# Kernel tuning notes

Measured on AMD Instinct MI355X. Metric: run time of the kernel, lower is better.

The kernel has to match this reference:

```python
import jax, jax.numpy as jnp
import numpy as np

B, T, H2, E, V = 64, 400, 1024, 256, 50000  # batch, src len, hidden*2, embed, vocab


def setup_inputs() -> dict:
    key = jax.random.key(0)
    ks = jax.random.split(key, 20)
    s = 0.02
    return {
        "input_ids": jax.random.randint(ks[0], (B, 1), 0, V),
        "pre_hidden": jax.random.normal(ks[1], (B, 1, H2), jnp.float32),
        "enc_out": jax.random.normal(ks[2], (B, T, H2), jnp.float32),
        "source_input": jax.random.randint(ks[3], (B, T), 0, V),
        "emb_table": jax.random.normal(ks[4], (V, E), jnp.float32) * s,
        "W_align": jax.random.normal(ks[5], (1, 2 * H2), jnp.float32) * s,
        "b_align": jnp.zeros((1,), jnp.float32),
        "W_ih": jax.random.normal(ks[6], (3 * H2, E), jnp.float32) * s,
        "W_hh": jax.random.normal(ks[7], (3 * H2, H2), jnp.float32) * s,
        "b_ih": jnp.zeros((3 * H2,), jnp.float32),
        "b_hh": jnp.zeros((3 * H2,), jnp.float32),
        "W_comb": jax.random.normal(ks[8], (E, H2 + E), jnp.float32) * s,
        "b_comb": jnp.zeros((E,), jnp.float32),
        "W_out": jax.random.normal(ks[9], (V, 2 * H2 + E), jnp.float32) * s,
        "b_out": jnp.zeros((V,), jnp.float32),
        "W_copy": jax.random.normal(ks[10], (H2, H2), jnp.float32) * s,
        "b_copy": jnp.zeros((H2,), jnp.float32),
    }


def reference(input_ids, pre_hidden, enc_out, source_input, emb_table,
              W_align, b_align, W_ih, W_hh, b_ih, b_hh,
              W_comb, b_comb, W_out, b_out, W_copy, b_copy):
    # embeddings: [B,1,E]  (dropout omitted: eval mode)
    emb = emb_table[input_ids[:, 0]][:, None, :]
    # Bahdanau-style alignment over source positions
    rep = jnp.broadcast_to(pre_hidden, (B, T, H2))
    scores = jnp.tanh(jnp.concatenate([enc_out, rep], axis=2) @ W_align.T + b_align)  # [B,T,1]
    attn = jax.nn.softmax(scores, axis=1)            # softmax over time, [B,T,1]
    attn_bt = attn[:, :, 0]                          # [B,T]
    attn_w = attn_bt[:, None, :]                     # [B,1,T] (returned shape)
    context = jnp.einsum("bt,bth->bh", attn_bt, enc_out)[:, None, :]  # [B,1,H2]
    # combine + relu -> GRU input
    new_in = jax.nn.relu(jnp.concatenate([emb, context], axis=2) @ W_comb.T + b_comb)  # [B,1,E]
    # single GRU step (torch gate order: r, z, n)
    x, h = new_in[:, 0], pre_hidden[:, 0]
    gi = x @ W_ih.T + b_ih
    gh = h @ W_hh.T + b_hh
    i_r, i_z, i_n = jnp.split(gi, 3, axis=1)
    h_r, h_z, h_n = jnp.split(gh, 3, axis=1)
    r = jax.nn.sigmoid(i_r + h_r)
    z = jax.nn.sigmoid(i_z + h_z)
    n = jnp.tanh(i_n + r * h_n)
    h_new = (1.0 - z) * n + z * h                    # [B,H2]
    current_hidden = h_new[:, None, :]               # [B,1,H2]
    # generation distribution
    feat = jnp.concatenate([emb[:, 0], context[:, 0], h_new], axis=1)  # [B,4H+E]
    gen = jax.nn.softmax(feat @ W_out.T + b_out, axis=1)               # [B,V]
    # copy attention weights (returned diagnostic)
    copy_a = jax.nn.sigmoid(enc_out @ W_copy.T + b_copy)               # [B,T,H2]
    copy_w = jax.nn.softmax(jnp.einsum("bth,bh->bt", copy_a, h_new), axis=1)
    # fused batched scatter-add replacing the per-example one-hot matmul loop
    pos = jnp.zeros((B, V), jnp.float32).at[jnp.arange(B)[:, None], source_input].add(attn_bt)
    out = gen + pos
    return out, current_hidden, attn_w, copy_w
```

## Files before the change

kernel.cpp:

```cpp
#include <hip/hip_runtime.h>
#include <hip/hip_bf16.h>
#include <cstddef>

#define BB 64
#define TT 400
#define H2 1024
#define EE 256
#define VV 50000
#define KF 2304
#define KC 1280

typedef _Float16 half8 __attribute__((ext_vector_type(8)));
typedef float f32x4 __attribute__((ext_vector_type(4)));

#define WS_SCORES   0
#define WS_ATTN     25600
#define WS_CONTEXT  51200
#define WS_X        116736
#define WS_HNEW     133120
#define WS_FEAT     198656
#define WS_SRAW     346112
#define WS_STATS    371712

#define OUT_MAIN    0
#define OUT_HID     3200000
#define OUT_ATTN    3265536
#define OUT_CPW     3291136

__device__ inline float sigm(float x){ return 1.f/(1.f + __expf(-x)); }

__global__ void k_scores(const float* __restrict__ enc, const float* __restrict__ Wa,
                         float* __restrict__ scores_raw){
  int wave = threadIdx.x >> 6, lane = threadIdx.x & 63;
  int row = blockIdx.x * 4 + wave;
  const float4* e4 = (const float4*)(enc + (size_t)row * H2);
  const float4* w4 = (const float4*)Wa;
  float acc = 0.f;
#pragma unroll
  for (int i = 0; i < 4; ++i){
    float4 e = e4[i*64 + lane], w = w4[i*64 + lane];
    acc += e.x*w.x + e.y*w.y + e.z*w.z + e.w*w.w;
  }
  for (int m = 32; m >= 1; m >>= 1) acc += __shfl_xor(acc, m, 64);
  if (lane == 0) scores_raw[row] = acc;
}

__global__ void k_attn(const float* __restrict__ scores_raw, const float* __restrict__ pre_hidden,
                       const float* __restrict__ Wa, const float* __restrict__ b_align,
                       float* __restrict__ attn_bt, float* __restrict__ attn_w_out){
  int b = blockIdx.x, t = threadIdx.x;
  __shared__ float red[256];
  const float4* p4 = (const float4*)(pre_hidden + (size_t)b * H2);
  const float4* w4 = (const float4*)(Wa + H2);
  float4 p = p4[t], w = w4[t];
  red[t] = p.x*w.x + p.y*w.y + p.z*w.z + p.w*w.w;
  __syncthreads();
  for (int s = 128; s > 0; s >>= 1){ if (t < s) red[t] += red[t+s]; __syncthreads(); }
  float phd = red[0] + b_align[0];
  __syncthreads();
  int t2 = t + 256;
  float v0 = -1e30f, v1 = -1e30f;
  if (t  < TT) v0 = tanhf(scores_raw[b*TT + t ] + phd);
  if (t2 < TT) v1 = tanhf(scores_raw[b*TT + t2] + phd);
  red[t] = fmaxf(v0, v1); __syncthreads();
  for (int s = 128; s > 0; s >>= 1){ if (t < s) red[t] = fmaxf(red[t], red[t+s]); __syncthreads(); }
  float M = red[0]; __syncthreads();
  float e0 = (t  < TT) ? __expf(v0 - M) : 0.f;
  float e1 = (t2 < TT) ? __expf(v1 - M) : 0.f;
  red[t] = e0 + e1; __syncthreads();
  for (int s = 128; s > 0; s >>= 1){ if (t < s) red[t] += red[t+s]; __syncthreads(); }
  float inv = 1.f / red[0];
  if (t < TT){ float a = e0*inv; attn_bt[b*TT+t] = a; attn_w_out[b*TT+t] = a; }
  if (t2 < TT){ float a = e1*inv; attn_bt[b*TT+t2] = a; attn_w_out[b*TT+t2] = a; }
}

__global__ void k_context(const float* __restrict__ enc, const float* __restrict__ attn_bt,
                          float* __restrict__ context){
  int bx = blockIdx.x;
  int b = bx >> 2;
  int h = (bx & 3) * 256 + threadIdx.x;
  const float* e = enc + (size_t)b * TT * H2 + h;
  const float* a = attn_bt + b * TT;
  float acc = 0.f;
  for (int t = 0; t < TT; t += 4){
    acc += a[t  ] * e[(size_t)(t  ) * H2];
    acc += a[t+1] * e[(size_t)(t+1) * H2];
    acc += a[t+2] * e[(size_t)(t+2) * H2];
    acc += a[t+3] * e[(size_t)(t+3) * H2];
  }
  context[b*H2 + h] = acc;
}

__global__ void k_newin(const int* __restrict__ input_ids, const float* __restrict__ emb_table,
                        const float* __restrict__ context, const float* __restrict__ W_comb,
                        const float* __restrict__ b_comb, float* __restrict__ x,
                        float* __restrict__ feat){
  int b = blockIdx.x, t = threadIdx.x;
  __shared__ float xs[KC];
  int id = input_ids[b];
  float ev = emb_table[(size_t)id * EE + t];
  xs[t] = ev; feat[b*KF + t] = ev;
#pragma unroll
  for (int q = 0; q < 4; ++q){
    float cv = context[b*H2 + q*256 + t];
    xs[EE + q*256 + t] = cv;
    feat[b*KF + EE + q*256 + t] = cv;
  }
  __syncthreads();
  const float4* w4 = (const float4*)(W_comb + (size_t)t * KC);
  const float4* x4 = (const float4*)xs;
  float acc = b_comb[t];
  for (int k = 0; k < KC/4; ++k){
    float4 w = w4[k], xv = x4[k];
    acc += w.x*xv.x + w.y*xv.y + w.z*xv.z + w.w*xv.w;
  }
  x[b*EE + t] = fmaxf(acc, 0.f);
}

__global__ void k_gru(const float* __restrict__ x, const float* __restrict__ pre_hidden,
                      const float* __restrict__ W_ih, const float* __restrict__ W_hh,
                      const float* __restrict__ b_ih, const float* __restrict__ b_hh,
                      float* __restrict__ h_new, float* __restrict__ feat,
                      float* __restrict__ cur_hid){
  int h = blockIdx.x, t = threadIdx.x;
  __shared__ float wi[768];
  __shared__ float wh[3072];
  wi[t      ] = W_ih[(size_t)(h        ) * EE + t];
  wi[256 + t] = W_ih[(size_t)(H2   + h ) * EE + t];
  wi[512 + t] = W_ih[(size_t)(2*H2 + h ) * EE + t];
#pragma unroll
  for (int q = 0; q < 4; ++q){
    wh[        q*256 + t] = W_hh[(size_t)(h       ) * H2 + q*256 + t];
    wh[1024 +  q*256 + t] = W_hh[(size_t)(H2  + h ) * H2 + q*256 + t];
    wh[2048 +  q*256 + t] = W_hh[(size_t)(2*H2 + h) * H2 + q*256 + t];
  }
  __syncthreads();
  int wave = t >> 6, lane = t & 63;
  float bir = b_ih[h], biz = b_ih[H2+h], bin = b_ih[2*H2+h];
  float bhr = b_hh[h], bhz = b_hh[H2+h], bhn = b_hh[2*H2+h];
  for (int bb = wave*16; bb < wave*16 + 16; ++bb){
    float air=0, aiz=0, ain=0, ahr=0, ahz=0, ahn=0;
#pragma unroll
    for (int i = 0; i < 4; ++i){
      float xv = x[bb*EE + i*64 + lane];
      air += xv * wi[      i*64 + lane];
      aiz += xv * wi[256 + i*64 + lane];
      ain += xv * wi[512 + i*64 + lane];
    }
#pragma unroll
    for (int i = 0; i < 16; ++i){
      float hv = pre_hidden[bb*H2 + i*64 + lane];
      ahr += hv * wh[        i*64 + lane];
      ahz += hv * wh[1024 +  i*64 + lane];
      ahn += hv * wh[2048 +  i*64 + lane];
    }
    for (int m = 32; m >= 1; m >>= 1){
      air += __shfl_xor(air, m, 64); aiz += __shfl_xor(aiz, m, 64); ain += __shfl_xor(ain, m, 64);
      ahr += __shfl_xor(ahr, m, 64); ahz += __shfl_xor(ahz, m, 64); ahn += __shfl_xor(ahn, m, 64);
    }
    if (lane == 0){
      float rg = sigm(air + bir + ahr + bhr);
      float zg = sigm(aiz + biz + ahz + bhz);
      float ng = tanhf(ain + bin + rg*(ahn + bhn));
      float hb = pre_hidden[bb*H2 + h];
      float hn = (1.f - zg)*ng + zg*hb;
      h_new[bb*H2 + h] = hn;
      cur_hid[bb*H2 + h] = hn;
      feat[bb*KF + KC + h] = hn;
    }
  }
}

__device__ inline void load16(const float* __restrict__ gp, float4* r){
  const float4* g4 = (const float4*)gp;
  r[0] = g4[0]; r[1] = g4[1]; r[2] = g4[2]; r[3] = g4[3];
}
__device__ inline void cvt16(const float4* r, _Float16* lp){
  half8 h0, h1;
  h0[0]=(_Float16)r[0].x; h0[1]=(_Float16)r[0].y; h0[2]=(_Float16)r[0].z; h0[3]=(_Float16)r[0].w;
  h0[4]=(_Float16)r[1].x; h0[5]=(_Float16)r[1].y; h0[6]=(_Float16)r[1].z; h0[7]=(_Float16)r[1].w;
  h1[0]=(_Float16)r[2].x; h1[1]=(_Float16)r[2].y; h1[2]=(_Float16)r[2].z; h1[3]=(_Float16)r[2].w;
  h1[4]=(_Float16)r[3].x; h1[5]=(_Float16)r[3].y; h1[6]=(_Float16)r[3].z; h1[7]=(_Float16)r[3].w;
  *(half8*)(lp)     = h0;
  *(half8*)(lp + 8) = h1;
}

__global__ __launch_bounds__(256) void k_gemm_copy(
    const float* __restrict__ A, const float* __restrict__ Wc,
    const float* __restrict__ b_copy, const float* __restrict__ h_new,
    float* __restrict__ s_raw){
  __shared__ _Float16 Ash[2][128*40];
  __shared__ _Float16 Bsh[2][128*40];
  int bx = blockIdx.x;
  int n0 = (bx & 7) * 128;
  int m0 = (bx >> 3) * 128;
  int tid = threadIdx.x;
  int lane = tid & 63, wave = tid >> 6;
  int wm = wave >> 1, wn = wave & 1;
  int quad = lane >> 4, r = lane & 15;
  int srow = tid >> 1, sc0 = (tid & 1) << 4;

  const float* Ap = A  + (size_t)(m0 + srow)*H2 + sc0;
  const float* Bp = Wc + (size_t)(n0 + srow)*H2 + sc0;

  f32x4 acc[4][4];
#pragma unroll
  for (int i = 0; i < 4; ++i)
#pragma unroll
    for (int j = 0; j < 4; ++j) acc[i][j] = (f32x4){0.f,0.f,0.f,0.f};

  float4 ra[4], rb[4];
  load16(Ap, ra); load16(Bp, rb);
  cvt16(ra, &Ash[0][srow*40 + sc0]); cvt16(rb, &Bsh[0][srow*40 + sc0]);
  load16(Ap + 32, ra); load16(Bp + 32, rb);
  __syncthreads();

  const int NT = H2/32;
  for (int kt = 0; kt < NT; ++kt){
    int cur = kt & 1;
    half8 af[4], bf[4];
#pragma unroll
    for (int i = 0; i < 4; ++i) af[i] = *(const half8*)&Ash[cur][(wm*64 + i*16 + r)*40 + quad*8];
#pragma unroll
    for (int j = 0; j < 4; ++j) bf[j] = *(const half8*)&Bsh[cur][(wn*64 + j*16 + r)*40 + quad*8];
    if (kt + 1 < NT){
      cvt16(ra, &Ash[cur^1][srow*40 + sc0]);
      cvt16(rb, &Bsh[cur^1][srow*40 + sc0]);
      if (kt + 2 < NT){
        load16(Ap + (kt+2)*32, ra);
        load16(Bp + (kt+2)*32, rb);
      }
    }
#pragma unroll
    for (int i = 0; i < 4; ++i)
#pragma unroll
      for (int j = 0; j < 4; ++j)
        acc[i][j] = __builtin_amdgcn_mfma_f32_16x16x32_f16(af[i], bf[j], acc[i][j], 0, 0, 0);
    __syncthreads();
  }
#pragma unroll
  for (int i = 0; i < 4; ++i){
#pragma unroll
    for (int rr = 0; rr < 4; ++rr){
      int m_loc = wm*64 + i*16 + quad*4 + rr;
      int m_g = m0 + m_loc;
      int b = m_g / TT;
      float v = 0.f;
#pragma unroll
      for (int j = 0; j < 4; ++j){
        int n_g = n0 + wn*64 + j*16 + r;
        float g = acc[i][j][rr] + b_copy[n_g];
        v += sigm(g) * h_new[b*H2 + n_g];
      }
      v += __shfl_xor(v, 1, 64); v += __shfl_xor(v, 2, 64);
      v += __shfl_xor(v, 4, 64); v += __shfl_xor(v, 8, 64);
      if (r == 0) atomicAdd(&s_raw[m_g], v);
    }
  }
}

__global__ void k_copysm(const float* __restrict__ s_raw, float* __restrict__ copy_w){
  int b = blockIdx.x, t = threadIdx.x;
  __shared__ float red[256];
  int t2 = t + 256;
  float v0 = (t  < TT) ? s_raw[b*TT + t ] : -1e30f;
  float v1 = (t2 < TT) ? s_raw[b*TT + t2] : -1e30f;
  red[t] = fmaxf(v0, v1); __syncthreads();
  for (int s = 128; s > 0; s >>= 1){ if (t < s) red[t] = fmaxf(red[t], red[t+s]); __syncthreads(); }
  float M = red[0]; __syncthreads();
  float e0 = (t  < TT) ? __expf(v0 - M) : 0.f;
  float e1 = (t2 < TT) ? __expf(v1 - M) : 0.f;
  red[t] = e0 + e1; __syncthreads();
  for (int s = 128; s > 0; s >>= 1){ if (t < s) red[t] += red[t+s]; __syncthreads(); }
  float inv = 1.f / red[0];
  if (t  < TT) copy_w[b*TT + t ] = e0 * inv;
  if (t2 < TT) copy_w[b*TT + t2] = e1 * inv;
}

__global__ __launch_bounds__(256) void k_gemm_out(
    const float* __restrict__ Wo, const float* __restrict__ feat,
    const float* __restrict__ b_out, float* __restrict__ logits){
  __shared__ __align__(16) char smem[33280];
  _Float16* AshB = (_Float16*)smem;
  _Float16* BshB = (_Float16*)(smem + 20480);
  float*    Csh  = (float*)smem;

  int m0 = blockIdx.x * 128;
  int tid = threadIdx.x;
  int lane = tid & 63, wave = tid >> 6;
  int wm = wave >> 1, wn = wave & 1;
  int quad = lane >> 4, r = lane & 15;

  f32x4 acc[4][2];
#pragma unroll
  for (int i = 0; i < 4; ++i)
#pragma unroll
    for (int j = 0; j < 2; ++j) acc[i][j] = (f32x4){0.f,0.f,0.f,0.f};

  int arow = tid >> 1, ac0 = (tid & 1) << 4;
  int arow_g = m0 + arow; if (arow_g >= VV) arow_g = VV - 1;
  const float* Ap = Wo + (size_t)arow_g * KF + ac0;
  const float* Bp = feat + (size_t)arow * KF + ac0;

  float4 ra[4], rb[4];
  load16(Ap, ra);
  if (tid < 128) load16(Bp, rb);
  cvt16(ra, &AshB[arow*40 + ac0]);
  if (tid < 128) cvt16(rb, &BshB[arow*40 + ac0]);
  load16(Ap + 32, ra);
  if (tid < 128) load16(Bp + 32, rb);
  __syncthreads();

  const int NT = KF/32;
  for (int kt = 0; kt < NT; ++kt){
    int cur = kt & 1;
    _Float16* Ash = AshB + cur*(128*40);
    _Float16* Bsh = BshB + cur*(64*40);
    half8 af[4], bf[2];
#pragma unroll
    for (int i = 0; i < 4; ++i) af[i] = *(const half8*)&Ash[(wm*64 + i*16 + r)*40 + quad*8];
#pragma unroll
    for (int j = 0; j < 2; ++j) bf[j] = *(const half8*)&Bsh[(wn*32 + j*16 + r)*40 + quad*8];
    if (kt + 1 < NT){
      int nxt = cur ^ 1;
      cvt16(ra, &AshB[nxt*(128*40) + arow*40 + ac0]);
      if (tid < 128) cvt16(rb, &BshB[nxt*(64*40) + arow*40 + ac0]);
      if (kt + 2 < NT){
        load16(Ap + (kt+2)*32, ra);
        if (tid < 128) load16(Bp + (kt+2)*32, rb);
      }
    }
#pragma unroll
    for (int i = 0; i < 4; ++i)
#pragma unroll
      for (int j = 0; j < 2; ++j)
        acc[i][j] = __builtin_amdgcn_mfma_f32_16x16x32_f16(af[i], bf[j], acc[i][j], 0, 0, 0);
    __syncthreads();
  }
#pragma unroll
  for (int i = 0; i < 4; ++i){
#pragma unroll
    for (int j = 0; j < 2; ++j){
#pragma unroll
      for (int rr = 0; rr < 4; ++rr){
        int m_loc = wm*64 + i*16 + quad*4 + rr;
        int n_loc = wn*32 + j*16 + r;
        int vg = m0 + m_loc;
        float bo = (vg < VV) ? b_out[vg] : 0.f;
        Csh[m_loc*65 + n_loc] = acc[i][j][rr] + bo;
      }
    }
  }
  __syncthreads();
  int vl = tid & 127, grp = tid >> 7;
  int vg = m0 + vl;
  if (vg < VV){
    for (int it = 0; it < 32; ++it){
      int brow = it*2 + grp;
      logits[(size_t)brow * VV + vg] = Csh[vl*65 + brow];
    }
  }
}

__global__ void k_gensm(const float* __restrict__ logits, float* __restrict__ stats){
  int b = blockIdx.x, t = threadIdx.x;
  __shared__ float red[256];
  const float* row = logits + (size_t)b * VV;
  float m = -1e30f;
  for (int v = t; v < VV; v += 256) m = fmaxf(m, row[v]);
  red[t] = m; __syncthreads();
  for (int s = 128; s > 0; s >>= 1){ if (t < s) red[t] = fmaxf(red[t], red[t+s]); __syncthreads(); }
  float M = red[0]; __syncthreads();
  float sum = 0.f;
  for (int v = t; v < VV; v += 256) sum += __expf(row[v] - M);
  red[t] = sum; __syncthreads();
  for (int s = 128; s > 0; s >>= 1){ if (t < s) red[t] += red[t+s]; __syncthreads(); }
  if (t == 0){ stats[b] = M; stats[64 + b] = 1.f / red[0]; }
}

__global__ void k_out(float* __restrict__ out, const float* __restrict__ stats){
  int idx4 = blockIdx.x * 256 + threadIdx.x;
  int base = idx4 * 4;
  int b = base / VV;
  float M = stats[b], inv = stats[64 + b];
  float4* p = (float4*)(out + base);
  float4 l = *p;
  l.x = __expf(l.x - M) * inv;
  l.y = __expf(l.y - M) * inv;
  l.z = __expf(l.z - M) * inv;
  l.w = __expf(l.w - M) * inv;
  *p = l;
}

__global__ void k_scatter(float* __restrict__ out, const int* __restrict__ src,
                          const float* __restrict__ attn_bt){
  int i = blockIdx.x * 256 + threadIdx.x;
  int b = i / TT;
  atomicAdd(&out[(size_t)b * VV + src[i]], attn_bt[i]);
}

extern "C" void kernel_launch(void* const* d_in, const int* in_sizes, int n_in,
                              void* d_out, int out_size, void* d_ws, size_t ws_size,
                              hipStream_t stream) {
  const int*   input_ids  = (const int*)  d_in[0];
  const float* pre_hidden = (const float*)d_in[1];
  const float* enc_out    = (const float*)d_in[2];
  const int*   source_in  = (const int*)  d_in[3];
  const float* emb_table  = (const float*)d_in[4];
  const float* W_align    = (const float*)d_in[5];
  const float* b_align    = (const float*)d_in[6];
  const float* W_ih       = (const float*)d_in[7];
  const float* W_hh       = (const float*)d_in[8];
  const float* b_ih       = (const float*)d_in[9];
  const float* b_hh       = (const float*)d_in[10];
  const float* W_comb     = (const float*)d_in[11];
  const float* b_comb     = (const float*)d_in[12];
  const float* W_out      = (const float*)d_in[13];
  const float* b_out      = (const float*)d_in[14];
  const float* W_copy     = (const float*)d_in[15];
  const float* b_copy     = (const float*)d_in[16];

  float* ws = (float*)d_ws;
  float* scores_raw = ws + WS_SCORES;
  float* attn_bt    = ws + WS_ATTN;
  float* context    = ws + WS_CONTEXT;
  float* x          = ws + WS_X;
  float* h_new      = ws + WS_HNEW;
  float* feat       = ws + WS_FEAT;
  float* s_raw      = ws + WS_SRAW;
  float* stats      = ws + WS_STATS;

  float* out        = (float*)d_out;
  float* out_hid    = out + OUT_HID;
  float* out_attn   = out + OUT_ATTN;
  float* out_cpw    = out + OUT_CPW;

  hipMemsetAsync(s_raw, 0, BB*TT*sizeof(float), stream);

  k_scores <<<BB*TT/4, 256, 0, stream>>>(enc_out, W_align, scores_raw);
  k_attn   <<<BB,      256, 0, stream>>>(scores_raw, pre_hidden, W_align, b_align, attn_bt, out_attn);
  k_context<<<BB*4,    256, 0, stream>>>(enc_out, attn_bt, context);
  k_newin  <<<BB,      256, 0, stream>>>(input_ids, emb_table, context, W_comb, b_comb, x, feat);
  k_gru    <<<H2,      256, 0, stream>>>(x, pre_hidden, W_ih, W_hh, b_ih, b_hh, h_new, feat, out_hid);
  k_gemm_copy<<<(BB*TT/128)*(H2/128), 256, 0, stream>>>(enc_out, W_copy, b_copy, h_new, s_raw);
  k_copysm <<<BB,      256, 0, stream>>>(s_raw, out_cpw);
  k_gemm_out<<<(VV + 127)/128, 256, 0, stream>>>(W_out, feat, b_out, out);
  k_gensm  <<<BB,      256, 0, stream>>>(out, stats);
  k_out    <<<BB*VV/1024, 256, 0, stream>>>(out, stats);
  k_scatter<<<BB*TT/256, 256, 0, stream>>>(out, source_in, attn_bt);
}
```

Before: 1.049 ms.

## Pre-convert copy GEMM operands to fp16, retile output GEMM, split softmax stats

enc_out is now converted to fp16 inside the scores kernel, and W_copy is converted by a new kernel, so the copy GEMM reads half-width operands instead of loading and converting fp32. The output GEMM tile shrinks from 128 to 64 vocab rows, which gives more blocks, and it gets a deeper three-stage register prefetch. The generation softmax statistics are split four ways per batch row and merged in k_out. Together these aim to cut memory traffic and raise parallelism, at the cost of an extra fp16 write of enc_out and added merge arithmetic.

After: 968.3 us. 1.08x faster.

```diff
diff --git a/kernel.cpp b/kernel.cpp
--- a/kernel.cpp
+++ b/kernel.cpp
@@ -11,6 +11,7 @@
 #define KC 1280
 
 typedef _Float16 half8 __attribute__((ext_vector_type(8)));
+typedef _Float16 half4 __attribute__((ext_vector_type(4)));
 typedef float f32x4 __attribute__((ext_vector_type(4)));
 
 #define WS_SCORES   0
@@ -21,6 +22,8 @@
 #define WS_FEAT     198656
 #define WS_SRAW     346112
 #define WS_STATS    371712
+#define WS_ENCH     372224
+#define WS_WCH      13479424
 
 #define OUT_MAIN    0
 #define OUT_HID     3200000
@@ -29,17 +32,30 @@
 
 __device__ inline float sigm(float x){ return 1.f/(1.f + __expf(-x)); }
 
+__global__ void k_cvt16(const float* __restrict__ src, _Float16* __restrict__ dst){
+  int i = blockIdx.x * 256 + threadIdx.x;
+  const float4* s4 = (const float4*)src;
+  float4 a = s4[i*2], b = s4[i*2+1];
+  half8 h;
+  h[0]=(_Float16)a.x; h[1]=(_Float16)a.y; h[2]=(_Float16)a.z; h[3]=(_Float16)a.w;
+  h[4]=(_Float16)b.x; h[5]=(_Float16)b.y; h[6]=(_Float16)b.z; h[7]=(_Float16)b.w;
+  *(half8*)(dst + (size_t)i*8) = h;
+}
+
 __global__ void k_scores(const float* __restrict__ enc, const float* __restrict__ Wa,
-                         float* __restrict__ scores_raw){
+                         float* __restrict__ scores_raw, _Float16* __restrict__ encH){
   int wave = threadIdx.x >> 6, lane = threadIdx.x & 63;
   int row = blockIdx.x * 4 + wave;
   const float4* e4 = (const float4*)(enc + (size_t)row * H2);
   const float4* w4 = (const float4*)Wa;
+  _Float16* eh = encH + (size_t)row * H2;
   float acc = 0.f;
 #pragma unroll
   for (int i = 0; i < 4; ++i){
     float4 e = e4[i*64 + lane], w = w4[i*64 + lane];
     acc += e.x*w.x + e.y*w.y + e.z*w.z + e.w*w.w;
+    half4 h; h[0]=(_Float16)e.x; h[1]=(_Float16)e.y; h[2]=(_Float16)e.z; h[3]=(_Float16)e.w;
+    *(half4*)(eh + (size_t)(i*64 + lane)*4) = h;
   }
   for (int m = 32; m >= 1; m >>= 1) acc += __shfl_xor(acc, m, 64);
   if (lane == 0) scores_raw[row] = acc;
@@ -171,22 +187,19 @@
   }
 }
 
-__device__ inline void load16(const float* __restrict__ gp, float4* r){
+__device__ inline void load8(const float* __restrict__ gp, float4* r){
   const float4* g4 = (const float4*)gp;
-  r[0] = g4[0]; r[1] = g4[1]; r[2] = g4[2]; r[3] = g4[3];
-}
-__device__ inline void cvt16(const float4* r, _Float16* lp){
-  half8 h0, h1;
-  h0[0]=(_Float16)r[0].x; h0[1]=(_Float16)r[0].y; h0[2]=(_Float16)r[0].z; h0[3]=(_Float16)r[0].w;
-  h0[4]=(_Float16)r[1].x; h0[5]=(_Float16)r[1].y; h0[6]=(_Float16)r[1].z; h0[7]=(_Float16)r[1].w;
-  h1[0]=(_Float16)r[2].x; h1[1]=(_Float16)r[2].y; h1[2]=(_Float16)r[2].z; h1[3]=(_Float16)r[2].w;
-  h1[4]=(_Float16)r[3].x; h1[5]=(_Float16)r[3].y; h1[6]=(_Float16)r[3].z; h1[7]=(_Float16)r[3].w;
-  *(half8*)(lp)     = h0;
-  *(half8*)(lp + 8) = h1;
+  r[0] = g4[0]; r[1] = g4[1];
+}
+__device__ inline void cvt8(const float4* r, _Float16* lp){
+  half8 h;
+  h[0]=(_Float16)r[0].x; h[1]=(_Float16)r[0].y; h[2]=(_Float16)r[0].z; h[3]=(_Float16)r[0].w;
+  h[4]=(_Float16)r[1].x; h[5]=(_Float16)r[1].y; h[6]=(_Float16)r[1].z; h[7]=(_Float16)r[1].w;
+  *(half8*)lp = h;
 }
 
 __global__ __launch_bounds__(256) void k_gemm_copy(
-    const float* __restrict__ A, const float* __restrict__ Wc,
+    const _Float16* __restrict__ A, const _Float16* __restrict__ Wc,
     const float* __restrict__ b_copy, const float* __restrict__ h_new,
     float* __restrict__ s_raw){
   __shared__ _Float16 Ash[2][128*40];
@@ -200,8 +213,8 @@
   int quad = lane >> 4, r = lane & 15;
   int srow = tid >> 1, sc0 = (tid & 1) << 4;
 
-  const float* Ap = A  + (size_t)(m0 + srow)*H2 + sc0;
-  const float* Bp = Wc + (size_t)(n0 + srow)*H2 + sc0;
+  const _Float16* Ap = A  + (size_t)(m0 + srow)*H2 + sc0;
+  const _Float16* Bp = Wc + (size_t)(n0 + srow)*H2 + sc0;
 
   f32x4 acc[4][4];
 #pragma unroll
@@ -209,10 +222,14 @@
 #pragma unroll
     for (int j = 0; j < 4; ++j) acc[i][j] = (f32x4){0.f,0.f,0.f,0.f};
 
-  float4 ra[4], rb[4];
-  load16(Ap, ra); load16(Bp, rb);
-  cvt16(ra, &Ash[0][srow*40 + sc0]); cvt16(rb, &Bsh[0][srow*40 + sc0]);
-  load16(Ap + 32, ra); load16(Bp + 32, rb);
+  {
+    half8 a0 = *(const half8*)(Ap), a1 = *(const half8*)(Ap+8);
+    half8 b0 = *(const half8*)(Bp), b1 = *(const half8*)(Bp+8);
+    *(half8*)&Ash[0][srow*40 + sc0] = a0; *(half8*)&Ash[0][srow*40 + sc0 + 8] = a1;
+    *(half8*)&Bsh[0][srow*40 + sc0] = b0; *(half8*)&Bsh[0][srow*40 + sc0 + 8] = b1;
+  }
+  half8 raL = *(const half8*)(Ap+32), raH = *(const half8*)(Ap+40);
+  half8 rbL = *(const half8*)(Bp+32), rbH = *(const half8*)(Bp+40);
   __syncthreads();
 
   const int NT = H2/32;
@@ -224,11 +241,13 @@
 #pragma unroll
     for (int j = 0; j < 4; ++j) bf[j] = *(const half8*)&Bsh[cur][(wn*64 + j*16 + r)*40 + quad*8];
     if (kt + 1 < NT){
-      cvt16(ra, &Ash[cur^1][srow*40 + sc0]);
-      cvt16(rb, &Bsh[cur^1][srow*40 + sc0]);
+      *(half8*)&Ash[cur^1][srow*40 + sc0]     = raL;
+      *(half8*)&Ash[cur^1][srow*40 + sc0 + 8] = raH;
+      *(half8*)&Bsh[cur^1][srow*40 + sc0]     = rbL;
+      *(half8*)&Bsh[cur^1][srow*40 + sc0 + 8] = rbH;
       if (kt + 2 < NT){
-        load16(Ap + (kt+2)*32, ra);
-        load16(Bp + (kt+2)*32, rb);
+        raL = *(const half8*)(Ap + (kt+2)*32); raH = *(const half8*)(Ap + (kt+2)*32 + 8);
+        rbL = *(const half8*)(Bp + (kt+2)*32); rbH = *(const half8*)(Bp + (kt+2)*32 + 8);
       }
     }
 #pragma unroll
@@ -280,70 +299,82 @@
 __global__ __launch_bounds__(256) void k_gemm_out(
     const float* __restrict__ Wo, const float* __restrict__ feat,
     const float* __restrict__ b_out, float* __restrict__ logits){
-  __shared__ __align__(16) char smem[33280];
+  __shared__ __align__(16) char smem[20480];
   _Float16* AshB = (_Float16*)smem;
-  _Float16* BshB = (_Float16*)(smem + 20480);
+  _Float16* BshB = (_Float16*)(smem + 10240);
   float*    Csh  = (float*)smem;
 
-  int m0 = blockIdx.x * 128;
+  int m0 = blockIdx.x * 64;
   int tid = threadIdx.x;
   int lane = tid & 63, wave = tid >> 6;
   int wm = wave >> 1, wn = wave & 1;
   int quad = lane >> 4, r = lane & 15;
 
-  f32x4 acc[4][2];
-#pragma unroll
-  for (int i = 0; i < 4; ++i)
+  f32x4 acc[2][2];
+#pragma unroll
+  for (int i = 0; i < 2; ++i)
 #pragma unroll
     for (int j = 0; j < 2; ++j) acc[i][j] = (f32x4){0.f,0.f,0.f,0.f};
 
-  int arow = tid >> 1, ac0 = (tid & 1) << 4;
+  int arow = tid >> 2, ac0 = (tid & 3) << 3;
   int arow_g = m0 + arow; if (arow_g >= VV) arow_g = VV - 1;
-  const float* Ap = Wo + (size_t)arow_g * KF + ac0;
-  const float* Bp = feat + (size_t)arow * KF + ac0;
-
-  float4 ra[4], rb[4];
-  load16(Ap, ra);
-  if (tid < 128) load16(Bp, rb);
-  cvt16(ra, &AshB[arow*40 + ac0]);
-  if (tid < 128) cvt16(rb, &BshB[arow*40 + ac0]);
-  load16(Ap + 32, ra);
-  if (tid < 128) load16(Bp + 32, rb);
+  const float* Ap = Wo  + (size_t)arow_g * KF + ac0;
+  const float* Bp = feat + (size_t)arow  * KF + ac0;
+
+  float4 a0[2], b0[2], aA[2], bA[2], aB[2], bB[2];
+  load8(Ap, a0); load8(Bp, b0);
+  cvt8(a0, &AshB[arow*40 + ac0]);
+  cvt8(b0, &BshB[arow*40 + ac0]);
+  load8(Ap + 32, aA); load8(Bp + 32, bA);
+  load8(Ap + 64, aB); load8(Bp + 64, bB);
   __syncthreads();
 
   const int NT = KF/32;
-  for (int kt = 0; kt < NT; ++kt){
-    int cur = kt & 1;
-    _Float16* Ash = AshB + cur*(128*40);
-    _Float16* Bsh = BshB + cur*(64*40);
-    half8 af[4], bf[2];
-#pragma unroll
-    for (int i = 0; i < 4; ++i) af[i] = *(const half8*)&Ash[(wm*64 + i*16 + r)*40 + quad*8];
-#pragma unroll
-    for (int j = 0; j < 2; ++j) bf[j] = *(const half8*)&Bsh[(wn*32 + j*16 + r)*40 + quad*8];
+  for (int kt = 0; kt < NT; kt += 2){
+    {
+      half8 af[2], bf[2];
+#pragma unroll
+      for (int i = 0; i < 2; ++i) af[i] = *(const half8*)&AshB[(wm*32 + i*16 + r)*40 + quad*8];
+#pragma unroll
+      for (int j = 0; j < 2; ++j) bf[j] = *(const half8*)&BshB[(wn*32 + j*16 + r)*40 + quad*8];
+      if (kt + 1 < NT){
+        cvt8(aA, &AshB[2560 + arow*40 + ac0]);
+        cvt8(bA, &BshB[2560 + arow*40 + ac0]);
+        if (kt + 3 < NT){ load8(Ap + (kt+3)*32, aA); load8(Bp + (kt+3)*32, bA); }
+      }
+#pragma unroll
+      for (int i = 0; i < 2; ++i)
+#pragma unroll
+        for (int j = 0; j < 2; ++j)
+          acc[i][j] = __builtin_amdgcn_mfma_f32_16x16x32_f16(af[i], bf[j], acc[i][j], 0, 0, 0);
+      __syncthreads();
+    }
     if (kt + 1 < NT){
-      int nxt = cur ^ 1;
-      cvt16(ra, &AshB[nxt*(128*40) + arow*40 + ac0]);
-      if (tid < 128) cvt16(rb, &BshB[nxt*(64*40) + arow*40 + ac0]);
+      half8 af[2], bf[2];
+#pragma unroll
+      for (int i = 0; i < 2; ++i) af[i] = *(const half8*)&AshB[2560 + (wm*32 + i*16 + r)*40 + quad*8];
+#pragma unroll
+      for (int j = 0; j < 2; ++j) bf[j] = *(const half8*)&BshB[2560 + (wn*32 + j*16 + r)*40 + quad*8];
       if (kt + 2 < NT){
-        load16(Ap + (kt+2)*32, ra);
-        if (tid < 128) load16(Bp + (kt+2)*32, rb);
+        cvt8(aB, &AshB[arow*40 + ac0]);
+        cvt8(bB, &BshB[arow*40 + ac0]);
+        if (kt + 4 < NT){ load8(Ap + (kt+4)*32, aB); load8(Bp + (kt+4)*32, bB); }
       }
-    }
-#pragma unroll
-    for (int i = 0; i < 4; ++i)
-#pragma unroll
-      for (int j = 0; j < 2; ++j)
-        acc[i][j] = __builtin_amdgcn_mfma_f32_16x16x32_f16(af[i], bf[j], acc[i][j], 0, 0, 0);
-    __syncthreads();
-  }
-#pragma unroll
-  for (int i = 0; i < 4; ++i){
+#pragma unroll
+      for (int i = 0; i < 2; ++i)
+#pragma unroll
+        for (int j = 0; j < 2; ++j)
+          acc[i][j] = __builtin_amdgcn_mfma_f32_16x16x32_f16(af[i], bf[j], acc[i][j], 0, 0, 0);
+      __syncthreads();
+    }
+  }
+#pragma unroll
+  for (int i = 0; i < 2; ++i){
 #pragma unroll
     for (int j = 0; j < 2; ++j){
 #pragma unroll
       for (int rr = 0; rr < 4; ++rr){
-        int m_loc = wm*64 + i*16 + quad*4 + rr;
+        int m_loc = wm*32 + i*16 + quad*4 + rr;
         int n_loc = wn*32 + j*16 + r;
         int vg = m0 + m_loc;
         float bo = (vg < VV) ? b_out[vg] : 0.f;
@@ -352,37 +383,45 @@
     }
   }
   __syncthreads();
-  int vl = tid & 127, grp = tid >> 7;
+  int vl = tid & 63, grp = tid >> 6;
   int vg = m0 + vl;
   if (vg < VV){
-    for (int it = 0; it < 32; ++it){
-      int brow = it*2 + grp;
+    for (int it = 0; it < 16; ++it){
+      int brow = it*4 + grp;
       logits[(size_t)brow * VV + vg] = Csh[vl*65 + brow];
     }
   }
 }
 
 __global__ void k_gensm(const float* __restrict__ logits, float* __restrict__ stats){
-  int b = blockIdx.x, t = threadIdx.x;
+  int bq = blockIdx.x;
+  int b = bq >> 2, q = bq & 3;
+  int t = threadIdx.x;
   __shared__ float red[256];
-  const float* row = logits + (size_t)b * VV;
+  const float* row = logits + (size_t)b * VV + q * 12500;
   float m = -1e30f;
-  for (int v = t; v < VV; v += 256) m = fmaxf(m, row[v]);
+  for (int v = t; v < 12500; v += 256) m = fmaxf(m, row[v]);
   red[t] = m; __syncthreads();
   for (int s = 128; s > 0; s >>= 1){ if (t < s) red[t] = fmaxf(red[t], red[t+s]); __syncthreads(); }
   float M = red[0]; __syncthreads();
   float sum = 0.f;
-  for (int v = t; v < VV; v += 256) sum += __expf(row[v] - M);
+  for (int v = t; v < 12500; v += 256) sum += __expf(row[v] - M);
   red[t] = sum; __syncthreads();
   for (int s = 128; s > 0; s >>= 1){ if (t < s) red[t] += red[t+s]; __syncthreads(); }
-  if (t == 0){ stats[b] = M; stats[64 + b] = 1.f / red[0]; }
+  if (t == 0){ stats[bq] = M; stats[256 + bq] = red[0]; }
 }
 
 __global__ void k_out(float* __restrict__ out, const float* __restrict__ stats){
   int idx4 = blockIdx.x * 256 + threadIdx.x;
   int base = idx4 * 4;
   int b = base / VV;
-  float M = stats[b], inv = stats[64 + b];
+  float m0 = stats[4*b], m1 = stats[4*b+1], m2 = stats[4*b+2], m3 = stats[4*b+3];
+  float M = fmaxf(fmaxf(m0, m1), fmaxf(m2, m3));
+  float s = stats[256 + 4*b  ] * __expf(m0 - M)
+          + stats[256 + 4*b+1] * __expf(m1 - M)
+          + stats[256 + 4*b+2] * __expf(m2 - M)
+          + stats[256 + 4*b+3] * __expf(m3 - M);
+  float inv = 1.f / s;
   float4* p = (float4*)(out + base);
   float4 l = *p;
   l.x = __expf(l.x - M) * inv;
@@ -429,6 +468,8 @@
   float* feat       = ws + WS_FEAT;
   float* s_raw      = ws + WS_SRAW;
   float* stats      = ws + WS_STATS;
+  _Float16* enc_h   = (_Float16*)(ws + WS_ENCH);
+  _Float16* wc_h    = (_Float16*)(ws + WS_WCH);
 
   float* out        = (float*)d_out;
   float* out_hid    = out + OUT_HID;
@@ -437,15 +478,16 @@
 
   hipMemsetAsync(s_raw, 0, BB*TT*sizeof(float), stream);
 
-  k_scores <<<BB*TT/4, 256, 0, stream>>>(enc_out, W_align, scores_raw);
+  k_cvt16  <<<H2*H2/8/256, 256, 0, stream>>>(W_copy, wc_h);
+  k_scores <<<BB*TT/4, 256, 0, stream>>>(enc_out, W_align, scores_raw, enc_h);
   k_attn   <<<BB,      256, 0, stream>>>(scores_raw, pre_hidden, W_align, b_align, attn_bt, out_attn);
   k_context<<<BB*4,    256, 0, stream>>>(enc_out, attn_bt, context);
   k_newin  <<<BB,      256, 0, stream>>>(input_ids, emb_table, context, W_comb, b_comb, x, feat);
   k_gru    <<<H2,      256, 0, stream>>>(x, pre_hidden, W_ih, W_hh, b_ih, b_hh, h_new, feat, out_hid);
-  k_gemm_copy<<<(BB*TT/128)*(H2/128), 256, 0, stream>>>(enc_out, W_copy, b_copy, h_new, s_raw);
+  k_gemm_copy<<<(BB*TT/128)*(H2/128), 256, 0, stream>>>(enc_h, wc_h, b_copy, h_new, s_raw);
   k_copysm <<<BB,      256, 0, stream>>>(s_raw, out_cpw);
-  k_gemm_out<<<(VV + 127)/128, 256, 0, stream>>>(W_out, feat, b_out, out);
-  k_gensm  <<<BB,      256, 0, stream>>>(out, stats);
+  k_gemm_out<<<(VV + 63)/64, 256, 0, stream>>>(W_out, feat, b_out, out);
+  k_gensm  <<<BB*4,    256, 0, stream>>>(out, stats);
   k_out    <<<BB*VV/1024, 256, 0, stream>>>(out, stats);
   k_scatter<<<BB*TT/256, 256, 0, stream>>>(out, source_in, attn_bt);
 }
```
